# Performance work log

Hardware: AMD Instinct MI355X
Metric: run time of the kernel (lower is better)

The kernel has to match this reference:

```python
import jax, jax.numpy as jnp
import numpy as np

CHUNK = 256
ROPE_BASE = 10000.0
EPS = 1e-6


def setup_inputs() -> dict:
    key = jax.random.key(0)
    ks = jax.random.split(key, 8)
    B, N, D, H, K = 4, 8192, 1024, 16, 4
    x = jax.random.normal(ks[0], (B, N, D), dtype=jnp.float32)
    norm_scale = jnp.ones((D,), dtype=jnp.float32)
    conv_w = jax.random.normal(ks[1], (D, 1, K), dtype=jnp.float32) * 0.2
    conv_b = jax.random.normal(ks[2], (D,), dtype=jnp.float32) * 0.02
    in_proj_w = jax.random.normal(ks[3], (D, 3 * D), dtype=jnp.float32) * 0.02
    dt_bias = jax.random.normal(ks[4], (D,), dtype=jnp.float32) * 0.5
    head_mix = jnp.eye(H, dtype=jnp.float32) + 0.02 * jax.random.normal(ks[5], (H, H), dtype=jnp.float32)
    out_proj_w = jax.random.normal(ks[6], (D, D), dtype=jnp.float32) * 0.02
    return {"x": x, "norm_scale": norm_scale, "conv_w": conv_w, "conv_b": conv_b,
            "in_proj_w": in_proj_w, "dt_bias": dt_bias, "head_mix": head_mix,
            "out_proj_w": out_proj_w}


def _rmsnorm(x, scale):
    xf = x.astype(jnp.float32)
    rms = jax.lax.rsqrt(jnp.mean(xf * xf, axis=-1, keepdims=True) + EPS)
    out = scale.astype(jnp.float32) * (xf * rms)
    return jnp.clip(out, -60000.0, 60000.0).astype(x.dtype)


def _rope(v, N, d_head, dtype):
    # v: (B, N, H, d_head); cos/sin: (N, d_head//2)
    half = d_head // 2
    inv_freq = 1.0 / (ROPE_BASE ** (jnp.arange(0, d_head, 2, dtype=jnp.float32) / d_head))
    freqs = jnp.arange(N, dtype=jnp.float32)[:, None] * inv_freq[None, :]
    cos = jnp.cos(freqs).astype(dtype)[None, :, None, :]
    sin = jnp.sin(freqs).astype(dtype)[None, :, None, :]
    v1, v2 = v[..., :half], v[..., half:]
    return jnp.concatenate([v1 * cos - v2 * sin, v1 * sin + v2 * cos], axis=-1)


def reference(x, norm_scale, conv_w, conv_b, in_proj_w, dt_bias, head_mix, out_proj_w):
    residual = x
    B, N, D = x.shape
    H = head_mix.shape[0]
    d_head = D // H
    xn = _rmsnorm(x, norm_scale)

    # depthwise causal conv: torch pads K-1 both sides then truncates to N -> left-pad only
    K = conv_w.shape[-1]
    xc = jax.lax.conv_general_dilated(
        xn.transpose(0, 2, 1), conv_w, window_strides=(1,), padding=[(K - 1, 0)],
        feature_group_count=D, dimension_numbers=("NCH", "OIH", "NCH"))
    xc = (xc + conv_b[None, :, None]).transpose(0, 2, 1)  # (B, N, D)
    xc = xc * jax.nn.sigmoid(xc)  # SiLU

    fused = xc @ in_proj_w  # (B, N, 3D)
    dt_raw, v, gate_raw = jnp.split(fused, 3, axis=-1)
    dt = jnp.clip(jax.nn.softplus(dt_raw.astype(jnp.float32) + dt_bias.astype(jnp.float32)),
                  0.001, 2.0).astype(dt_raw.dtype)
    gate = jax.nn.sigmoid(gate_raw)
    log_alpha = -dt.astype(jnp.float32)

    v_rot = _rope(v.reshape(B, N, H, d_head), N, d_head, x.dtype).reshape(B, N, D)
    v_in = (v_rot * dt).astype(jnp.float32)

    # pad to multiple of CHUNK (static)
    pad = (-N) % CHUNK
    if pad:
        v_in = jnp.pad(v_in, ((0, 0), (0, pad), (0, 0)))
        log_alpha = jnp.pad(log_alpha, ((0, 0), (0, pad), (0, 0)))
    Np = N + pad
    nc = Np // CHUNK
    v_ch = v_in.reshape(B, nc, CHUNK, D)
    la_ch = log_alpha.reshape(B, nc, CHUNK, D)

    # intra-chunk stabilized cumulative scan
    L = jnp.clip(jnp.cumsum(la_ch, axis=2), -20.0, 0.0)
    L_max = jnp.max(L, axis=2, keepdims=True)
    L_st = L - L_max
    cum_scaled = jnp.cumsum(jnp.exp(-L_st) * v_ch, axis=2)
    chunk_out = jnp.exp(L_st) * cum_scaled  # (B, nc, CHUNK, D)

    if nc > 1:
        # inter-chunk carry, fully parallel
        bdecay = L[:, :, -1, :]            # (B, nc, D)
        bout = chunk_out[:, :, -1, :]      # (B, nc, D)
        cum_decay = jnp.clip(jnp.cumsum(bdecay, axis=1), -80.0, 0.0)
        stab = jnp.max(cum_decay, axis=1, keepdims=True)
        ncd = jnp.clip(cum_decay - stab, -20.0, 0.0)
        seeds = bout * jnp.exp(-ncd)
        shifted = jnp.pad(seeds[:, :-1], ((0, 0), (1, 0), (0, 0)))
        carries = jnp.cumsum(shifted, axis=1) * jnp.exp(ncd)  # (B, nc, D)
        final = chunk_out + carries[:, :, None, :] * jnp.exp(L)
    else:
        final = chunk_out
    final = final.astype(x.dtype).reshape(B, Np, D)[:, :N, :]

    v_mix = jnp.einsum("bnhd,hm->bnmd", final.reshape(B, N, H, d_head), head_mix)
    final = v_mix.reshape(B, N, D)
    out = (final * gate) @ out_proj_w
    return residual + out
```

## Files before the change

kernel.cpp:

```cpp
#include <hip/hip_runtime.h>

#define TOK 32768
#define DMODEL 1024
#define NSEQ 8192
#define NCHK 32
#define CHUNKC 256
#define KDIM 1024
#define NKT (KDIM / 32)
#define LOG2E 1.44269504f

typedef __attribute__((ext_vector_type(8))) short bf16x8;
typedef __attribute__((ext_vector_type(4))) float f32x4;

__device__ __forceinline__ unsigned short f2bf(float f) {
  unsigned u = __float_as_uint(f);
  u += 0x7fffu + ((u >> 16) & 1u);
  return (unsigned short)(u >> 16);
}
__device__ __forceinline__ float bf2f(unsigned short h) {
  return __uint_as_float(((unsigned)h) << 16);
}
__device__ __forceinline__ float sigm(float x) {
  return __builtin_amdgcn_rcpf(1.f + exp2f(-LOG2E * x));
}

typedef __attribute__((address_space(3))) unsigned int lds_u32_t;
typedef const __attribute__((address_space(1))) unsigned int glb_u32_t;

__device__ __forceinline__ void gl_lds16(const void* g, void* l) {
  __builtin_amdgcn_global_load_lds((glb_u32_t*)g, (lds_u32_t*)l, 16, 0, 0);
}

__global__ __launch_bounds__(256) void transpose_bf16_k(const float* __restrict__ in,
                                                        unsigned short* __restrict__ out,
                                                        int R, int C) {
  __shared__ float tile[32][33];
  const int c0 = blockIdx.x * 32, r0 = blockIdx.y * 32;
  const int tx = threadIdx.x, ty = threadIdx.y;
#pragma unroll
  for (int i = 0; i < 32; i += 8)
    tile[ty + i][tx] = in[(long)(r0 + ty + i) * C + c0 + tx];
  __syncthreads();
#pragma unroll
  for (int i = 0; i < 32; i += 8)
    out[(long)(c0 + ty + i) * R + r0 + tx] = f2bf(tile[tx][ty + i]);
}

__global__ __launch_bounds__(256) void ropetab_k(float2* __restrict__ tab) {
  const int i = blockIdx.x * 256 + threadIdx.x;
  const int f = i & 31, n = i >> 5;
  const float invf = exp2f(-(float)f * (13.287712379549449f / 32.0f));
  const float ang = (float)n * invf;
  tab[i] = make_float2(cosf(ang), sinf(ang));
}

__global__ __launch_bounds__(256) void rmsconv_k(const float* __restrict__ x,
                                                 const float* __restrict__ scale,
                                                 const float* __restrict__ w,
                                                 const float* __restrict__ cb,
                                                 unsigned short* __restrict__ xc) {
  __shared__ float xs[11][1024];
  __shared__ float red[4];
  const int t = threadIdx.x;
  const long row0 = (long)blockIdx.x * 8;
  const bool seqstart = ((row0 & (NSEQ - 1)) == 0);
  const float4 sc = ((const float4*)scale)[t];
  for (int i = 0; i < 11; ++i) {
    if (i < 3 && seqstart) {
      ((float4*)xs[i])[t] = make_float4(0.f, 0.f, 0.f, 0.f);
      continue;
    }
    const long r = row0 - 3 + i;
    const float4 v = ((const float4*)(x + r * DMODEL))[t];
    float ss = v.x * v.x + v.y * v.y + v.z * v.z + v.w * v.w;
#pragma unroll
    for (int off = 32; off > 0; off >>= 1) ss += __shfl_down(ss, off);
    if ((t & 63) == 0) red[t >> 6] = ss;
    __syncthreads();
    const float tot = red[0] + red[1] + red[2] + red[3];
    const float rr = rsqrtf(tot * (1.0f / DMODEL) + 1e-6f);
    float4 o;
    o.x = fminf(fmaxf(v.x * rr * sc.x, -60000.f), 60000.f);
    o.y = fminf(fmaxf(v.y * rr * sc.y, -60000.f), 60000.f);
    o.z = fminf(fmaxf(v.z * rr * sc.z, -60000.f), 60000.f);
    o.w = fminf(fmaxf(v.w * rr * sc.w, -60000.f), 60000.f);
    ((float4*)xs[i])[t] = o;
    __syncthreads();
  }
  __syncthreads();
  const int d0 = t * 4;
  float wl[4][4];
#pragma unroll
  for (int j = 0; j < 4; ++j) {
    const float4 t4 = *(const float4*)(w + (d0 + j) * 4);
    wl[j][0] = t4.x; wl[j][1] = t4.y; wl[j][2] = t4.z; wl[j][3] = t4.w;
  }
  const float4 cb4 = ((const float4*)cb)[t];
#pragma unroll
  for (int orow = 0; orow < 8; ++orow) {
    float o[4] = {0.f, 0.f, 0.f, 0.f};
#pragma unroll
    for (int k = 0; k < 4; ++k) {
      const float4 xv = ((const float4*)xs[orow + k])[t];
      o[0] += xv.x * wl[0][k]; o[1] += xv.y * wl[1][k];
      o[2] += xv.z * wl[2][k]; o[3] += xv.w * wl[3][k];
    }
    ushort4 st;
    { const float a = o[0] + cb4.x; st.x = f2bf(a * sigm(a)); }
    { const float a = o[1] + cb4.y; st.y = f2bf(a * sigm(a)); }
    { const float a = o[2] + cb4.z; st.z = f2bf(a * sigm(a)); }
    { const float a = o[3] + cb4.w; st.w = f2bf(a * sigm(a)); }
    *(ushort4*)(xc + (row0 + orow) * DMODEL + d0) = st;
  }
}

template <int EPI, int NBN, int SBN>
__global__ __launch_bounds__(256) void gemm_bt(const unsigned short* __restrict__ A,
                                               const unsigned short* __restrict__ BT,
                                               unsigned short* __restrict__ ob,
                                               float* __restrict__ of,
                                               const float* __restrict__ resid) {
  __shared__ unsigned short As[3][128 * 32];
  __shared__ unsigned short Bs[3][128 * 32];
  const int tid = threadIdx.x;
  const int l = tid & 63;
  const int w = tid >> 6;
  const int wr = w >> 1, wc = w & 1;
  constexpr int NC = (EPI == 0) ? 3072 : 1024;

  constexpr int BPS = 4 * SBN;
  constexpr int NBNS = NBN / SBN;
  const int lin = blockIdx.y * NBN + blockIdx.x;
  const int xcd = lin & 7;
  const int g = lin >> 3;
  const int s = g / BPS;
  const int r = g - s * BPS;
  const int bmo = r / SBN;
  const int bno = r - bmo * SBN;
  const int bmS = s / NBNS;
  const int bnS = s - bmS * NBNS;
  const int bm = xcd * 32 + bmS * 4 + bmo;
  const int bn = bnS * SBN + bno;

  f32x4 acc[4][4];
#pragma unroll
  for (int m = 0; m < 4; ++m)
#pragma unroll
    for (int n = 0; n < 4; ++n) acc[m][n] = {0.f, 0.f, 0.f, 0.f};

  const int srcc = (((l & 3) ^ ((l >> 3) & 3)) * 8);
  const unsigned short* aGb = A + ((long)(bm * 128 + w * 16 + (l >> 2))) * KDIM + srcc;
  const unsigned short* bGb = BT + ((long)(bn * 128 + w * 16 + (l >> 2))) * KDIM + srcc;
  const int ldso = (w * 16) * 32;

#define STAGE(buf, k0)                                          \
  {                                                             \
    gl_lds16(aGb + (k0),               &As[buf][ldso]);         \
    gl_lds16(aGb + (k0) + 64 * KDIM,   &As[buf][ldso + 2048]);  \
    gl_lds16(bGb + (k0),               &Bs[buf][ldso]);         \
    gl_lds16(bGb + (k0) + 64 * KDIM,   &Bs[buf][ldso + 2048]);  \
  }

  const int eoff = (((l >> 4) ^ ((l >> 1) & 3)) * 8);
  const int arow = (wr * 64 + (l & 15)) * 32 + eoff;
  const int brow = (wc * 64 + (l & 15)) * 32 + eoff;

  auto compute = [&](int cur) {
    const unsigned short* Ab = &As[cur][0];
    const unsigned short* Bb = &Bs[cur][0];
    bf16x8 af[4], bfr[4];
#pragma unroll
    for (int m = 0; m < 4; ++m) af[m] = *(const bf16x8*)&Ab[arow + m * 512];
#pragma unroll
    for (int n = 0; n < 4; ++n) bfr[n] = *(const bf16x8*)&Bb[brow + n * 512];
    __builtin_amdgcn_s_setprio(1);
#pragma unroll
    for (int m = 0; m < 4; ++m)
#pragma unroll
      for (int n = 0; n < 4; ++n)
        acc[m][n] = __builtin_amdgcn_mfma_f32_16x16x32_bf16(af[m], bfr[n], acc[m][n], 0, 0, 0);
    __builtin_amdgcn_s_setprio(0);
  };

  STAGE(0, 0);
  STAGE(1, 32);
  asm volatile("s_waitcnt vmcnt(4)" ::: "memory");
  int cur = 0, nxt = 2;
  for (int t = 0; t < NKT - 2; ++t) {
    __builtin_amdgcn_s_barrier();
    __builtin_amdgcn_sched_barrier(0);
    STAGE(nxt, (t + 2) * 32);
    compute(cur);
    asm volatile("s_waitcnt vmcnt(4)" ::: "memory");
    cur = (cur == 2) ? 0 : cur + 1;
    nxt = (nxt == 2) ? 0 : nxt + 1;
  }
  __builtin_amdgcn_s_barrier();
  __builtin_amdgcn_sched_barrier(0);
  compute(cur);
  asm volatile("s_waitcnt vmcnt(0)" ::: "memory");
  cur = (cur == 2) ? 0 : cur + 1;
  __builtin_amdgcn_s_barrier();
  __builtin_amdgcn_sched_barrier(0);
  compute(cur);
#undef STAGE

  const int rbase = bm * 128 + wr * 64;
  const int cbase = bn * 128 + wc * 64;
  const int lr4 = (l >> 4) * 4;
  const int lc16 = l & 15;

  if constexpr (EPI == 0) {
#pragma unroll
    for (int m = 0; m < 4; ++m)
#pragma unroll
      for (int n = 0; n < 4; ++n) {
        const int col = cbase + n * 16 + lc16;
#pragma unroll
        for (int j2 = 0; j2 < 4; ++j2) {
          const int row = rbase + m * 16 + lr4 + j2;
          ob[(long)row * NC + col] = f2bf(acc[m][n][j2]);
        }
      }
  } else {
#pragma unroll
    for (int m = 0; m < 4; ++m)
#pragma unroll
      for (int n = 0; n < 4; ++n) {
        const int col = cbase + n * 16 + lc16;
#pragma unroll
        for (int j2 = 0; j2 < 4; ++j2) {
          const int row = rbase + m * 16 + lr4 + j2;
          const long o = (long)row * NC + col;
          of[o] = resid[o] + acc[m][n][j2];
        }
      }
  }
}

__global__ __launch_bounds__(256) void scan1_k(const unsigned short* __restrict__ fu,
                                               const float* __restrict__ dt_bias,
                                               const float2* __restrict__ tab,
                                               float* __restrict__ Llast,
                                               float* __restrict__ bout) {
  const int idx = blockIdx.x * 256 + threadIdx.x;
  const int d = idx & 1023;
  const int ch = (idx >> 10) & 31;
  const int b = idx >> 15;
  const long base = ((long)b * NSEQ + ch * CHUNKC) * 3072 + d;
  const float bias = dt_bias[d];
  const int f = d & 31;
  const bool hi = (d & 32) != 0;
  const int po = hi ? -32 : 32;
  float run = 0.f, s = 0.f, L = 0.f;
#pragma unroll 4
  for (int c = 0; c < CHUNKC; ++c) {
    const long o = base + (long)c * 3072;
    const float a = bf2f(fu[o]) + bias;
    const float e2 = exp2f(-LOG2E * fabsf(a));
    const float sp = fmaxf(a, 0.f) + 0.69314718f * log2f(1.f + e2);
    const float dtv = fminf(fmaxf(sp, 0.001f), 2.0f);
    const float own = bf2f(fu[o + 1024]);
    const float oth = bf2f(fu[o + 1024 + po]);
    const float2 cs = tab[(ch * CHUNKC + c) * 32 + f];
    const float vr = own * cs.x + (hi ? oth * cs.y : -oth * cs.y);
    run -= dtv;
    L = fminf(fmaxf(run, -20.f), 0.f);
    s += exp2f(-LOG2E * L) * (vr * dtv);
  }
  Llast[idx] = L;
  bout[idx] = exp2f(LOG2E * L) * s;
}

__global__ __launch_bounds__(256) void scan2_k(const float* __restrict__ Llast,
                                               const float* __restrict__ bout,
                                               float* __restrict__ carry) {
  const int idx = blockIdx.x * 256 + threadIdx.x;
  const int d = idx & 1023;
  const int b = idx >> 10;
  const long base = (long)b * (NCHK * DMODEL) + d;
  float cd[NCHK];
  float run = 0.f, stab = -1e30f;
#pragma unroll
  for (int ch = 0; ch < NCHK; ++ch) {
    run += Llast[base + ch * DMODEL];
    cd[ch] = fminf(fmaxf(run, -80.f), 0.f);
    stab = fmaxf(stab, cd[ch]);
  }
  float acc = 0.f;
#pragma unroll
  for (int ch = 0; ch < NCHK; ++ch) {
    const float ncd = fminf(fmaxf(cd[ch] - stab, -20.f), 0.f);
    carry[base + ch * DMODEL] = acc * exp2f(LOG2E * ncd);
    acc += bout[base + ch * DMODEL] * exp2f(-LOG2E * ncd);
  }
}

__global__ __launch_bounds__(256) void scan3_k(unsigned short* fu,
                                               const float* __restrict__ dt_bias,
                                               const float2* __restrict__ tab,
                                               const float* __restrict__ carry) {
  const int idx = blockIdx.x * 256 + threadIdx.x;
  const int d = idx & 1023;
  const int ch = (idx >> 10) & 31;
  const int b = idx >> 15;
  const long base = ((long)b * NSEQ + ch * CHUNKC) * 3072 + d;
  const float bias = dt_bias[d];
  const int f = d & 31;
  const bool hi = (d & 32) != 0;
  const int po = hi ? -32 : 32;
  const float ce = carry[idx];
  float run = 0.f, s = 0.f;
#pragma unroll 4
  for (int c = 0; c < CHUNKC; ++c) {
    const long o = base + (long)c * 3072;
    const float a = bf2f(fu[o]) + bias;
    const float e2 = exp2f(-LOG2E * fabsf(a));
    const float sp = fmaxf(a, 0.f) + 0.69314718f * log2f(1.f + e2);
    const float dtv = fminf(fmaxf(sp, 0.001f), 2.0f);
    const float own = bf2f(fu[o + 1024]);
    const float oth = bf2f(fu[o + 1024 + po]);
    const float2 cs = tab[(ch * CHUNKC + c) * 32 + f];
    const float vr = own * cs.x + (hi ? oth * cs.y : -oth * cs.y);
    run -= dtv;
    const float L = fminf(fmaxf(run, -20.f), 0.f);
    s += exp2f(-LOG2E * L) * (vr * dtv);
    fu[o + 1024] = f2bf(exp2f(LOG2E * L) * (s + ce));
  }
}

__global__ __launch_bounds__(256) void headmix_k(const unsigned short* __restrict__ fu,
                                                 const float* __restrict__ hm,
                                                 unsigned short* __restrict__ A2) {
  __shared__ float mixs[256];
  const int t = threadIdx.x;
  mixs[t] = hm[t];
  __syncthreads();
  const long row = (long)blockIdx.x * 4 + (t >> 6);
  const int dd = t & 63;
  const unsigned short* fv0 = fu + row * 3072 + 1024 + dd;
  const unsigned short* gv0 = fu + row * 3072 + 2048 + dd;
  float fv[16];
#pragma unroll
  for (int h = 0; h < 16; ++h) fv[h] = bf2f(fv0[h * 64]);
#pragma unroll
  for (int m = 0; m < 16; ++m) {
    float o = 0.f;
#pragma unroll
    for (int h = 0; h < 16; ++h) o += fv[h] * mixs[h * 16 + m];
    A2[row * DMODEL + m * 64 + dd] = f2bf(o * sigm(bf2f(gv0[m * 64])));
  }
}

extern "C" void kernel_launch(void* const* d_in, const int* in_sizes, int n_in,
                              void* d_out, int out_size, void* d_ws, size_t ws_size,
                              hipStream_t stream) {
  const float* x        = (const float*)d_in[0];
  const float* nscale   = (const float*)d_in[1];
  const float* conv_w   = (const float*)d_in[2];
  const float* conv_b   = (const float*)d_in[3];
  const float* in_proj  = (const float*)d_in[4];
  const float* dt_bias  = (const float*)d_in[5];
  const float* head_mix = (const float*)d_in[6];
  const float* out_proj = (const float*)d_in[7];
  float* out = (float*)d_out;

  char* p = (char*)d_ws;
  unsigned short* W1T = (unsigned short*)p; p += (size_t)3072 * 1024 * 2;
  unsigned short* W2T = (unsigned short*)p; p += (size_t)1024 * 1024 * 2;
  float2* tab  = (float2*)p; p += (size_t)NSEQ * 32 * sizeof(float2);
  float* Llast = (float*)p;  p += (size_t)131072 * 4;
  float* bout  = (float*)p;  p += (size_t)131072 * 4;
  float* carry = (float*)p;  p += (size_t)131072 * 4;
  unsigned short* fusedb = (unsigned short*)p; p += (size_t)TOK * 3072 * 2;
  unsigned short* xc     = (unsigned short*)p; p += (size_t)TOK * DMODEL * 2;

  transpose_bf16_k<<<dim3(96, 32), dim3(32, 8), 0, stream>>>(in_proj, W1T, 1024, 3072);
  transpose_bf16_k<<<dim3(32, 32), dim3(32, 8), 0, stream>>>(out_proj, W2T, 1024, 1024);
  ropetab_k<<<1024, 256, 0, stream>>>(tab);
  rmsconv_k<<<TOK / 8, 256, 0, stream>>>(x, nscale, conv_w, conv_b, xc);

  gemm_bt<0, 24, 6><<<dim3(24, 256), 256, 0, stream>>>(xc, W1T, fusedb, nullptr, nullptr);
  scan1_k<<<512, 256, 0, stream>>>(fusedb, dt_bias, tab, Llast, bout);
  scan2_k<<<16, 256, 0, stream>>>(Llast, bout, carry);
  scan3_k<<<512, 256, 0, stream>>>(fusedb, dt_bias, tab, carry);
  headmix_k<<<TOK / 4, 256, 0, stream>>>(fusedb, head_mix, xc );
  gemm_bt<1, 8, 8><<<dim3(8, 256), 256, 0, stream>>>(xc, W2T, nullptr, out, x);
}
```

Baseline: 648.9 us.

## Widen GEMM block tile to 128x256 with per-wave 128x64 subtiles

Both GEMM instances change from a 128x128 block tile with a 2x2 wave layout to a 128x256 tile, where each of the four waves computes all 128 rows against its own 64-column slice. Each wave now holds 8x4 MFMA accumulators and loads 8 A fragments per k-step, which raises arithmetic intensity per LDS read and halves the number of blocks. The cost is higher register pressure (128 accumulator floats per lane), more LDS (B buffers doubled), and fewer blocks, which hurts occupancy and tail balance, especially for the 1024-wide second GEMM (only 4 column blocks).

```diff
diff --git a/kernel.cpp b/kernel.cpp
--- a/kernel.cpp
+++ b/kernel.cpp
@@ -121,11 +121,10 @@
                                                float* __restrict__ of,
                                                const float* __restrict__ resid) {
   __shared__ unsigned short As[3][128 * 32];
-  __shared__ unsigned short Bs[3][128 * 32];
+  __shared__ unsigned short Bs[3][256 * 32];
   const int tid = threadIdx.x;
   const int l = tid & 63;
   const int w = tid >> 6;
-  const int wr = w >> 1, wc = w & 1;
   constexpr int NC = (EPI == 0) ? 3072 : 1024;
 
   constexpr int BPS = 4 * SBN;
@@ -142,40 +141,43 @@
   const int bm = xcd * 32 + bmS * 4 + bmo;
   const int bn = bnS * SBN + bno;
 
-  f32x4 acc[4][4];
-#pragma unroll
-  for (int m = 0; m < 4; ++m)
+  f32x4 acc[8][4];
+#pragma unroll
+  for (int m = 0; m < 8; ++m)
 #pragma unroll
     for (int n = 0; n < 4; ++n) acc[m][n] = {0.f, 0.f, 0.f, 0.f};
 
   const int srcc = (((l & 3) ^ ((l >> 3) & 3)) * 8);
-  const unsigned short* aGb = A + ((long)(bm * 128 + w * 16 + (l >> 2))) * KDIM + srcc;
-  const unsigned short* bGb = BT + ((long)(bn * 128 + w * 16 + (l >> 2))) * KDIM + srcc;
-  const int ldso = (w * 16) * 32;
-
-#define STAGE(buf, k0)                                          \
-  {                                                             \
-    gl_lds16(aGb + (k0),               &As[buf][ldso]);         \
-    gl_lds16(aGb + (k0) + 64 * KDIM,   &As[buf][ldso + 2048]);  \
-    gl_lds16(bGb + (k0),               &Bs[buf][ldso]);         \
-    gl_lds16(bGb + (k0) + 64 * KDIM,   &Bs[buf][ldso + 2048]);  \
+  const unsigned short* aG0 = A + ((long)(bm * 128 + w * 32 + (l >> 2))) * KDIM + srcc;
+  const unsigned short* bG0 = BT + ((long)(bn * 256 + w * 64 + (l >> 2))) * KDIM + srcc;
+  const int aLo = (w * 32) * 32;
+  const int bLo = (w * 64) * 32;
+
+#define STAGE(buf, k0)                                           \
+  {                                                              \
+    gl_lds16(aG0 + (k0),             &As[buf][aLo]);             \
+    gl_lds16(aG0 + (k0) + 16 * KDIM, &As[buf][aLo + 512]);       \
+    gl_lds16(bG0 + (k0),             &Bs[buf][bLo]);             \
+    gl_lds16(bG0 + (k0) + 16 * KDIM, &Bs[buf][bLo + 512]);       \
+    gl_lds16(bG0 + (k0) + 32 * KDIM, &Bs[buf][bLo + 1024]);      \
+    gl_lds16(bG0 + (k0) + 48 * KDIM, &Bs[buf][bLo + 1536]);      \
   }
 
   const int eoff = (((l >> 4) ^ ((l >> 1) & 3)) * 8);
-  const int arow = (wr * 64 + (l & 15)) * 32 + eoff;
-  const int brow = (wc * 64 + (l & 15)) * 32 + eoff;
+  const int arow0 = (l & 15) * 32 + eoff;
+  const int brow0 = (w * 64 + (l & 15)) * 32 + eoff;
 
   auto compute = [&](int cur) {
     const unsigned short* Ab = &As[cur][0];
     const unsigned short* Bb = &Bs[cur][0];
-    bf16x8 af[4], bfr[4];
-#pragma unroll
-    for (int m = 0; m < 4; ++m) af[m] = *(const bf16x8*)&Ab[arow + m * 512];
-#pragma unroll
-    for (int n = 0; n < 4; ++n) bfr[n] = *(const bf16x8*)&Bb[brow + n * 512];
+    bf16x8 af[8], bfr[4];
+#pragma unroll
+    for (int m = 0; m < 8; ++m) af[m] = *(const bf16x8*)&Ab[arow0 + m * 512];
+#pragma unroll
+    for (int n = 0; n < 4; ++n) bfr[n] = *(const bf16x8*)&Bb[brow0 + n * 512];
     __builtin_amdgcn_s_setprio(1);
 #pragma unroll
-    for (int m = 0; m < 4; ++m)
+    for (int m = 0; m < 8; ++m)
 #pragma unroll
       for (int n = 0; n < 4; ++n)
         acc[m][n] = __builtin_amdgcn_mfma_f32_16x16x32_bf16(af[m], bfr[n], acc[m][n], 0, 0, 0);
@@ -184,14 +186,14 @@
 
   STAGE(0, 0);
   STAGE(1, 32);
-  asm volatile("s_waitcnt vmcnt(4)" ::: "memory");
+  asm volatile("s_waitcnt vmcnt(6)" ::: "memory");
   int cur = 0, nxt = 2;
   for (int t = 0; t < NKT - 2; ++t) {
     __builtin_amdgcn_s_barrier();
     __builtin_amdgcn_sched_barrier(0);
     STAGE(nxt, (t + 2) * 32);
     compute(cur);
-    asm volatile("s_waitcnt vmcnt(4)" ::: "memory");
+    asm volatile("s_waitcnt vmcnt(6)" ::: "memory");
     cur = (cur == 2) ? 0 : cur + 1;
     nxt = (nxt == 2) ? 0 : nxt + 1;
   }
@@ -205,14 +207,14 @@
   compute(cur);
 #undef STAGE
 
-  const int rbase = bm * 128 + wr * 64;
-  const int cbase = bn * 128 + wc * 64;
+  const int rbase = bm * 128;
+  const int cbase = bn * 256 + w * 64;
   const int lr4 = (l >> 4) * 4;
   const int lc16 = l & 15;
 
   if constexpr (EPI == 0) {
 #pragma unroll
-    for (int m = 0; m < 4; ++m)
+    for (int m = 0; m < 8; ++m)
 #pragma unroll
       for (int n = 0; n < 4; ++n) {
         const int col = cbase + n * 16 + lc16;
@@ -224,7 +226,7 @@
       }
   } else {
 #pragma unroll
-    for (int m = 0; m < 4; ++m)
+    for (int m = 0; m < 8; ++m)
 #pragma unroll
       for (int n = 0; n < 4; ++n) {
         const int col = cbase + n * 16 + lc16;
@@ -380,10 +382,10 @@
   ropetab_k<<<1024, 256, 0, stream>>>(tab);
   rmsconv_k<<<TOK / 8, 256, 0, stream>>>(x, nscale, conv_w, conv_b, xc);
 
-  gemm_bt<0, 24, 6><<<dim3(24, 256), 256, 0, stream>>>(xc, W1T, fusedb, nullptr, nullptr);
+  gemm_bt<0, 12, 6><<<dim3(12, 256), 256, 0, stream>>>(xc, W1T, fusedb, nullptr, nullptr);
   scan1_k<<<512, 256, 0, stream>>>(fusedb, dt_bias, tab, Llast, bout);
   scan2_k<<<16, 256, 0, stream>>>(Llast, bout, carry);
   scan3_k<<<512, 256, 0, stream>>>(fusedb, dt_bias, tab, carry);
   headmix_k<<<TOK / 4, 256, 0, stream>>>(fusedb, head_mix, xc );
-  gemm_bt<1, 8, 8><<<dim3(8, 256), 256, 0, stream>>>(xc, W2T, nullptr, out, x);
-}
+  gemm_bt<1, 4, 4><<<dim3(4, 256), 256, 0, stream>>>(xc, W2T, nullptr, out, x);
+}
```

Measured after the change: 626.8 us. -3.4%, faster.
